# Optimization experiments

Measured on AMD Instinct MI355X. Metric: run time of the kernel, lower is better.

## Reference

```python
import jax, jax.numpy as jnp
import numpy as np

B, S, D, H = 8, 1024, 768, 12
DH = D // H  # 64
EPS = 1e-12
NEG_INF = -1e30


def setup_inputs() -> dict:
    key = jax.random.key(0)
    ks = jax.random.split(key, 12)
    s = 0.02
    return {
        "hidden_states": jax.random.normal(ks[0], (B, S, D), jnp.float32),
        "attention_mask": jax.random.randint(ks[1], (B, 1, 1, S), 0, 2, jnp.int32),
        "Wq": jax.random.normal(ks[2], (D, D), jnp.float32) * s,
        "bq": jnp.zeros((D,), jnp.float32),
        "Wk": jax.random.normal(ks[3], (D, D), jnp.float32) * s,
        "bk": jnp.zeros((D,), jnp.float32),
        "Wv": jax.random.normal(ks[4], (D, D), jnp.float32) * s,
        "bv": jnp.zeros((D,), jnp.float32),
        "Wo": jax.random.normal(ks[5], (D, D), jnp.float32) * s,
        "bo": jnp.zeros((D,), jnp.float32),
        "ln_g": jnp.ones((D,), jnp.float32),
        "ln_b": jnp.zeros((D,), jnp.float32),
    }


def _split_heads(x):
    # [B,S,D] -> [B,H,S,DH]
    return x.reshape(B, S, H, DH).transpose(0, 2, 1, 3)


def reference(hidden_states, attention_mask, Wq, bq, Wk, bk, Wv, bv, Wo, bo, ln_g, ln_b):
    q = _split_heads(hidden_states @ Wq.T + bq)
    k = _split_heads(hidden_states @ Wk.T + bk)
    v = _split_heads(hidden_states @ Wv.T + bv)

    # scores: [B,H,S,S]
    scores = jnp.einsum("bhqd,bhkd->bhqk", q, k) / jnp.float32(np.sqrt(DH))
    mask0 = attention_mask == 0  # [B,1,1,S], broadcasts over heads/queries
    scores = jnp.where(mask0, NEG_INF, scores)
    probs = jax.nn.softmax(scores, axis=-1)
    # post-softmax masking (as in source)
    probs = jnp.where(mask0, 0.0, probs)

    ctx = jnp.einsum("bhqk,bhkd->bhqd", probs, v)
    ctx = ctx.transpose(0, 2, 1, 3).reshape(B, S, D)

    # BertSelfOutput: dense + residual + LayerNorm
    h = ctx @ Wo.T + bo + hidden_states
    mu = jnp.mean(h, axis=-1, keepdims=True)
    var = jnp.mean((h - mu) ** 2, axis=-1, keepdims=True)
    out = (h - mu) * jax.lax.rsqrt(var + EPS) * ln_g + ln_b
    return out, probs
```

## Files before the change

kernel.cpp:

```cpp
#include <hip/hip_runtime.h>

#define B_ 8
#define S_ 1024
#define D_ 768
#define H_ 12
#define DH_ 64

typedef __attribute__((ext_vector_type(8))) short short8;
typedef __attribute__((ext_vector_type(4))) short short4v;
typedef __attribute__((ext_vector_type(4))) float float4v;
typedef __attribute__((ext_vector_type(8))) __bf16 bf16x8;

static __device__ __forceinline__ short f2bf(float f) {
  union { float f; unsigned u; } v; v.f = f;
  unsigned r = v.u + 0x7fffu + ((v.u >> 16) & 1u);
  return (short)(r >> 16);
}

static __device__ __forceinline__ float4v mfma16(const short* ap, const short* bp, float4v c) {
  bf16x8 a = *(const bf16x8*)ap;
  bf16x8 b = *(const bf16x8*)bp;
  return __builtin_amdgcn_mfma_f32_16x16x32_bf16(a, b, c, 0, 0, 0);
}

__global__ __launch_bounds__(256) void cvt_bf16(const float* __restrict__ src,
                                                short* __restrict__ dst, int n4) {
  int i = blockIdx.x * 256 + threadIdx.x;
  if (i < n4) {
    float4v v = ((const float4v*)src)[i];
    short4v o;
    o.x = f2bf(v.x); o.y = f2bf(v.y); o.z = f2bf(v.z); o.w = f2bf(v.w);
    ((short4v*)dst)[i] = o;
  }
}

#define AST 56

__global__ __launch_bounds__(256) void gemm_qkv(const short* __restrict__ A,
                                                const short* __restrict__ Bw,
                                                const float* __restrict__ bq,
                                                const float* __restrict__ bk,
                                                const float* __restrict__ bv,
                                                short* __restrict__ Qb,
                                                short* __restrict__ Kb,
                                                short* __restrict__ Vtb) {
  __shared__ short As[128][AST];
  __shared__ short Bs[128][AST];
  int m0 = blockIdx.x * 128, n0 = blockIdx.y * 128;
  int t = threadIdx.x;
  int w = t >> 6, lane = t & 63;
  int wm = (w >> 1) * 64, wn = (w & 1) * 64;
  int lr = lane & 15, lk = (lane >> 4) * 8;
  int sr = t >> 2, sc = (t & 3) * 8;

  float4v acc[4][4] = {};

  for (int k0 = 0; k0 < 768; k0 += 32) {
    *(short8*)&As[sr][sc]      = *(const short8*)&A[(size_t)(m0 + sr) * 768 + k0 + sc];
    *(short8*)&As[sr + 64][sc] = *(const short8*)&A[(size_t)(m0 + sr + 64) * 768 + k0 + sc];
    *(short8*)&Bs[sr][sc]      = *(const short8*)&Bw[(size_t)(n0 + sr) * 768 + k0 + sc];
    *(short8*)&Bs[sr + 64][sc] = *(const short8*)&Bw[(size_t)(n0 + sr + 64) * 768 + k0 + sc];
    __syncthreads();
    short8 a[4], b[4];
#pragma unroll
    for (int i = 0; i < 4; i++) a[i] = *(const short8*)&As[wm + i * 16 + lr][lk];
#pragma unroll
    for (int j = 0; j < 4; j++) b[j] = *(const short8*)&Bs[wn + j * 16 + lr][lk];
#pragma unroll
    for (int i = 0; i < 4; i++)
#pragma unroll
      for (int j = 0; j < 4; j++)
        acc[i][j] = mfma16((const short*)&a[i], (const short*)&b[j], acc[i][j]);
    __syncthreads();
  }

  int proj = n0 / 768;
  int nloc0 = n0 - proj * 768;
  const float* bias = (proj == 0) ? bq : ((proj == 1) ? bk : bv);
#pragma unroll
  for (int j = 0; j < 4; j++) {
    int gn = nloc0 + wn + j * 16 + lr;
    int hh = gn >> 6, dh = gn & 63;
    float bb = bias[gn];
#pragma unroll
    for (int i = 0; i < 4; i++) {
      int gm0 = m0 + wm + i * 16 + ((lane >> 4) << 2);
#pragma unroll
      for (int jj = 0; jj < 4; jj++) {
        int r = gm0 + jj;
        int bidx = r >> 10, s = r & 1023;
        short val = f2bf(acc[i][j][jj] + bb);
        if (proj == 2)
          Vtb[(((size_t)bidx * 12 + hh) * 64 + dh) * 1024 + s] = val;
        else {
          short* dst = (proj == 0) ? Qb : Kb;
          dst[(((size_t)bidx * 12 + hh) * 1024 + s) * 64 + dh] = val;
        }
      }
    }
  }
}

__global__ __launch_bounds__(256) void attn_fused(const short* __restrict__ Qb,
                                                  const short* __restrict__ Kb,
                                                  const short* __restrict__ Vtb,
                                                  const int* __restrict__ amask,
                                                  float* __restrict__ probs,
                                                  short* __restrict__ ctxb) {
  __shared__ short P[16][1032];
  __shared__ float redmax[4][16];
  __shared__ float redsum[4][16];
  __shared__ float ctxp[4][16][64];

  int bh = blockIdx.y;
  int b = bh / 12, h = bh - b * 12;
  int q0 = blockIdx.x * 16;
  const short* Qp = Qb + ((size_t)bh * 1024 + q0) * 64;
  const short* Kp = Kb + (size_t)bh * 1024 * 64;
  const short* Vp = Vtb + (size_t)bh * 64 * 1024;
  const int* mb = amask + b * 1024;

  int t = threadIdx.x, w = t >> 6, lane = t & 63;
  int lr = lane & 15, lk = (lane >> 4) * 8;

  short8 aq0 = *(const short8*)&Qp[lr * 64 + lk];
  short8 aq1 = *(const short8*)&Qp[lr * 64 + 32 + lk];

  float4v acc[16] = {};
#pragma unroll
  for (int nt = 0; nt < 16; nt++) {
    const short* kp = Kp + (size_t)(w * 256 + nt * 16 + lr) * 64;
    short8 b0 = *(const short8*)&kp[lk];
    short8 b1 = *(const short8*)&kp[32 + lk];
    acc[nt] = mfma16((const short*)&aq0, (const short*)&b0, acc[nt]);
    acc[nt] = mfma16((const short*)&aq1, (const short*)&b1, acc[nt]);
  }

  unsigned mbits = 0;
#pragma unroll
  for (int nt = 0; nt < 16; nt++)
    mbits |= (mb[w * 256 + nt * 16 + lr] != 0 ? 1u : 0u) << nt;

  float mx[4] = {-1e30f, -1e30f, -1e30f, -1e30f};
#pragma unroll
  for (int nt = 0; nt < 16; nt++)
#pragma unroll
    for (int j = 0; j < 4; j++) {
      float s = acc[nt][j] * 0.125f;
      if (!((mbits >> nt) & 1)) s = -1e30f;
      acc[nt][j] = s;
      mx[j] = fmaxf(mx[j], s);
    }
#pragma unroll
  for (int j = 0; j < 4; j++) {
#pragma unroll
    for (int off = 1; off < 16; off <<= 1) mx[j] = fmaxf(mx[j], __shfl_xor(mx[j], off));
  }
  if (lr == 0) {
#pragma unroll
    for (int j = 0; j < 4; j++) redmax[w][(lane >> 4) * 4 + j] = mx[j];
  }
  __syncthreads();
  float gmx[4];
#pragma unroll
  for (int j = 0; j < 4; j++) {
    int r = (lane >> 4) * 4 + j;
    gmx[j] = fmaxf(fmaxf(redmax[0][r], redmax[1][r]), fmaxf(redmax[2][r], redmax[3][r]));
  }

  float sm[4] = {0.f, 0.f, 0.f, 0.f};
#pragma unroll
  for (int nt = 0; nt < 16; nt++)
#pragma unroll
    for (int j = 0; j < 4; j++) {
      float p = ((mbits >> nt) & 1) ? __expf(acc[nt][j] - gmx[j]) : 0.f;
      acc[nt][j] = p;
      sm[j] += p;
    }
#pragma unroll
  for (int j = 0; j < 4; j++) {
#pragma unroll
    for (int off = 1; off < 16; off <<= 1) sm[j] += __shfl_xor(sm[j], off);
  }
  if (lr == 0) {
#pragma unroll
    for (int j = 0; j < 4; j++) redsum[w][(lane >> 4) * 4 + j] = sm[j];
  }
  __syncthreads();
  float inv[4];
#pragma unroll
  for (int j = 0; j < 4; j++) {
    int r = (lane >> 4) * 4 + j;
    float s = redsum[0][r] + redsum[1][r] + redsum[2][r] + redsum[3][r];
    inv[j] = (s > 0.f) ? 1.f / s : 0.f;
  }

  size_t pbase = ((size_t)bh * 1024 + q0) * 1024;
#pragma unroll
  for (int nt = 0; nt < 16; nt++) {
    int col = w * 256 + nt * 16 + lr;
#pragma unroll
    for (int j = 0; j < 4; j++) {
      int row = (lane >> 4) * 4 + j;
      float pv = acc[nt][j] * inv[j];
      probs[pbase + (size_t)row * 1024 + col] = pv;
      P[row][col] = f2bf(pv);
    }
  }
  __syncthreads();

  float4v c[4] = {};
#pragma unroll
  for (int ks = 0; ks < 8; ks++) {
    int kbase = w * 256 + ks * 32;
    short8 ap = *(const short8*)&P[lr][kbase + lk];
#pragma unroll
    for (int n2 = 0; n2 < 4; n2++) {
      short8 bvv = *(const short8*)&Vp[(size_t)(n2 * 16 + lr) * 1024 + kbase + lk];
      c[n2] = mfma16((const short*)&ap, (const short*)&bvv, c[n2]);
    }
  }
#pragma unroll
  for (int n2 = 0; n2 < 4; n2++)
#pragma unroll
    for (int j = 0; j < 4; j++)
      ctxp[w][(lane >> 4) * 4 + j][n2 * 16 + lr] = c[n2][j];
  __syncthreads();

#pragma unroll
  for (int u = 0; u < 4; u++) {
    int o = t * 4 + u;
    int row = o >> 6, dh = o & 63;
    float s = ctxp[0][row][dh] + ctxp[1][row][dh] + ctxp[2][row][dh] + ctxp[3][row][dh];
    ctxb[((size_t)(b * 1024 + q0 + row)) * 768 + h * 64 + dh] = f2bf(s);
  }
}

__global__ __launch_bounds__(256) void gemm_o(const short* __restrict__ A,
                                              const short* __restrict__ Bw,
                                              const float* __restrict__ bo,
                                              const float* __restrict__ hidden,
                                              float* __restrict__ hout) {
  __shared__ short As[128][AST];
  __shared__ short Bs[128][AST];
  int m0 = blockIdx.x * 128, n0 = blockIdx.y * 128;
  int t = threadIdx.x;
  int w = t >> 6, lane = t & 63;
  int wm = (w >> 1) * 64, wn = (w & 1) * 64;
  int lr = lane & 15, lk = (lane >> 4) * 8;
  int sr = t >> 2, sc = (t & 3) * 8;

  float4v acc[4][4] = {};

  for (int k0 = 0; k0 < 768; k0 += 32) {
    *(short8*)&As[sr][sc]      = *(const short8*)&A[(size_t)(m0 + sr) * 768 + k0 + sc];
    *(short8*)&As[sr + 64][sc] = *(const short8*)&A[(size_t)(m0 + sr + 64) * 768 + k0 + sc];
    *(short8*)&Bs[sr][sc]      = *(const short8*)&Bw[(size_t)(n0 + sr) * 768 + k0 + sc];
    *(short8*)&Bs[sr + 64][sc] = *(const short8*)&Bw[(size_t)(n0 + sr + 64) * 768 + k0 + sc];
    __syncthreads();
    short8 a[4], b[4];
#pragma unroll
    for (int i = 0; i < 4; i++) a[i] = *(const short8*)&As[wm + i * 16 + lr][lk];
#pragma unroll
    for (int j = 0; j < 4; j++) b[j] = *(const short8*)&Bs[wn + j * 16 + lr][lk];
#pragma unroll
    for (int i = 0; i < 4; i++)
#pragma unroll
      for (int j = 0; j < 4; j++)
        acc[i][j] = mfma16((const short*)&a[i], (const short*)&b[j], acc[i][j]);
    __syncthreads();
  }

#pragma unroll
  for (int j = 0; j < 4; j++) {
    int gn = n0 + wn + j * 16 + lr;
    float bb = bo[gn];
#pragma unroll
    for (int i = 0; i < 4; i++) {
      int gm0 = m0 + wm + i * 16 + ((lane >> 4) << 2);
#pragma unroll
      for (int jj = 0; jj < 4; jj++) {
        int r = gm0 + jj;
        size_t idx = (size_t)r * 768 + gn;
        hout[idx] = acc[i][j][jj] + bb + hidden[idx];
      }
    }
  }
}

__global__ __launch_bounds__(256) void lnorm(const float* __restrict__ h,
                                             const float* __restrict__ g,
                                             const float* __restrict__ be,
                                             float* __restrict__ out) {
  int row = blockIdx.x;
  const float* x = h + (size_t)row * 768;
  int t = threadIdx.x;
  float v0 = x[t], v1 = x[t + 256], v2 = x[t + 512];
  float s = v0 + v1 + v2;
#pragma unroll
  for (int off = 1; off < 64; off <<= 1) s += __shfl_xor(s, off);
  __shared__ float r1[4], r2[4];
  if ((t & 63) == 0) r1[t >> 6] = s;
  __syncthreads();
  float mean = (r1[0] + r1[1] + r1[2] + r1[3]) * (1.f / 768.f);
  float d0 = v0 - mean, d1 = v1 - mean, d2 = v2 - mean;
  float q = d0 * d0 + d1 * d1 + d2 * d2;
#pragma unroll
  for (int off = 1; off < 64; off <<= 1) q += __shfl_xor(q, off);
  if ((t & 63) == 0) r2[t >> 6] = q;
  __syncthreads();
  float var = (r2[0] + r2[1] + r2[2] + r2[3]) * (1.f / 768.f);
  float rr = rsqrtf(var + 1e-12f);
  size_t o = (size_t)row * 768;
  out[o + t]       = d0 * rr * g[t] + be[t];
  out[o + t + 256] = d1 * rr * g[t + 256] + be[t + 256];
  out[o + t + 512] = d2 * rr * g[t + 512] + be[t + 512];
}

extern "C" void kernel_launch(void* const* d_in, const int* in_sizes, int n_in,
                              void* d_out, int out_size, void* d_ws, size_t ws_size,
                              hipStream_t stream) {
  const float* hs    = (const float*)d_in[0];
  const int*   amask = (const int*)d_in[1];
  const float* Wq    = (const float*)d_in[2];
  const float* bq    = (const float*)d_in[3];
  const float* Wk    = (const float*)d_in[4];
  const float* bk    = (const float*)d_in[5];
  const float* Wv    = (const float*)d_in[6];
  const float* bv    = (const float*)d_in[7];
  const float* Wo    = (const float*)d_in[8];
  const float* bo    = (const float*)d_in[9];
  const float* lng   = (const float*)d_in[10];
  const float* lnb   = (const float*)d_in[11];

  char* wsp = (char*)d_ws;
  const size_t NTOK = (size_t)B_ * S_;
  short* hsb  = (short*)wsp; wsp += NTOK * D_ * 2;
  short* wqkv = (short*)wsp; wsp += (size_t)3 * D_ * D_ * 2;
  short* wob  = (short*)wsp; wsp += (size_t)D_ * D_ * 2;
  short* Qb   = (short*)wsp; wsp += NTOK * D_ * 2;
  short* Kb   = (short*)wsp; wsp += NTOK * D_ * 2;
  short* Vtb  = (short*)wsp; wsp += NTOK * D_ * 2;
  short* ctxb = (short*)wsp; wsp += NTOK * D_ * 2;
  float* hbuf = (float*)wsp; wsp += NTOK * D_ * 4;

  float* out   = (float*)d_out;
  float* probs = out + NTOK * D_;

  int n4hs = (int)(NTOK * D_ / 4);
  cvt_bf16<<<dim3((n4hs + 255) / 256), dim3(256), 0, stream>>>(hs, hsb, n4hs);
  int n4w = D_ * D_ / 4;
  dim3 wg((n4w + 255) / 256);
  cvt_bf16<<<wg, dim3(256), 0, stream>>>(Wq, wqkv, n4w);
  cvt_bf16<<<wg, dim3(256), 0, stream>>>(Wk, wqkv + (size_t)D_ * D_, n4w);
  cvt_bf16<<<wg, dim3(256), 0, stream>>>(Wv, wqkv + (size_t)2 * D_ * D_, n4w);
  cvt_bf16<<<wg, dim3(256), 0, stream>>>(Wo, wob, n4w);

  gemm_qkv<<<dim3(64, 18), dim3(256), 0, stream>>>(hsb, wqkv, bq, bk, bv, Qb, Kb, Vtb);
  attn_fused<<<dim3(S_ / 16, B_ * H_), dim3(256), 0, stream>>>(Qb, Kb, Vtb, amask, probs, ctxb);
  gemm_o<<<dim3(64, 6), dim3(256), 0, stream>>>(ctxb, wob, bo, hs, hbuf);
  lnorm<<<dim3(8192), dim3(256), 0, stream>>>(hbuf, lng, lnb, out);
}
```

Before: 758.9 us.

## Use direct global-to-LDS loads in GEMMs and coalesce output stores via LDS staging

Both projection GEMMs now load A and B tiles with global_load_lds (16-byte direct-to-LDS transfers) into unpadded 32-wide LDS tiles, which removes the register round-trip. The QKV epilogue stages results in shared memory so Q/K/V^T are written with 16-byte coalesced stores instead of scattered 2-byte stores. The attention kernel writes probs as float4 rows read back from the bf16 P buffer, and writes ctx as packed 4-element stores. The unpadded LDS tiles may cause bank conflicts. Probs are now rounded to bf16 precision before being stored, which changes output accuracy.

```diff
diff --git a/kernel.cpp b/kernel.cpp
--- a/kernel.cpp
+++ b/kernel.cpp
@@ -16,11 +16,21 @@
   unsigned r = v.u + 0x7fffu + ((v.u >> 16) & 1u);
   return (short)(r >> 16);
 }
+static __device__ __forceinline__ float bf2f(short s) {
+  union { unsigned u; float f; } v; v.u = ((unsigned)(unsigned short)s) << 16;
+  return v.f;
+}
 
 static __device__ __forceinline__ float4v mfma16(const short* ap, const short* bp, float4v c) {
   bf16x8 a = *(const bf16x8*)ap;
   bf16x8 b = *(const bf16x8*)bp;
   return __builtin_amdgcn_mfma_f32_16x16x32_bf16(a, b, c, 0, 0, 0);
+}
+
+typedef const __attribute__((address_space(1))) unsigned gu32;
+typedef __attribute__((address_space(3))) unsigned lu32;
+static __device__ __forceinline__ void gload16(const void* g, void* l) {
+  __builtin_amdgcn_global_load_lds((gu32*)g, (lu32*)l, 16, 0, 0);
 }
 
 __global__ __launch_bounds__(256) void cvt_bf16(const float* __restrict__ src,
@@ -34,8 +44,6 @@
   }
 }
 
-#define AST 56
-
 __global__ __launch_bounds__(256) void gemm_qkv(const short* __restrict__ A,
                                                 const short* __restrict__ Bw,
                                                 const float* __restrict__ bq,
@@ -44,22 +52,27 @@
                                                 short* __restrict__ Qb,
                                                 short* __restrict__ Kb,
                                                 short* __restrict__ Vtb) {
-  __shared__ short As[128][AST];
-  __shared__ short Bs[128][AST];
+  __shared__ char smem[34816];
+  short (*As)[32] = (short(*)[32])smem;
+  short (*Bs)[32] = (short(*)[32])(smem + 8192);
+  short (*Cs)[136] = (short(*)[136])smem;
+
   int m0 = blockIdx.x * 128, n0 = blockIdx.y * 128;
-  int t = threadIdx.x;
-  int w = t >> 6, lane = t & 63;
+  int t = threadIdx.x, w = t >> 6, lane = t & 63;
   int wm = (w >> 1) * 64, wn = (w & 1) * 64;
   int lr = lane & 15, lk = (lane >> 4) * 8;
-  int sr = t >> 2, sc = (t & 3) * 8;
+
+  const short* gA = A + (size_t)(m0 + w * 32 + (lane >> 2)) * 768 + (lane & 3) * 8;
+  const short* gB = Bw + (size_t)(n0 + w * 32 + (lane >> 2)) * 768 + (lane & 3) * 8;
 
   float4v acc[4][4] = {};
 
   for (int k0 = 0; k0 < 768; k0 += 32) {
-    *(short8*)&As[sr][sc]      = *(const short8*)&A[(size_t)(m0 + sr) * 768 + k0 + sc];
-    *(short8*)&As[sr + 64][sc] = *(const short8*)&A[(size_t)(m0 + sr + 64) * 768 + k0 + sc];
-    *(short8*)&Bs[sr][sc]      = *(const short8*)&Bw[(size_t)(n0 + sr) * 768 + k0 + sc];
-    *(short8*)&Bs[sr + 64][sc] = *(const short8*)&Bw[(size_t)(n0 + sr + 64) * 768 + k0 + sc];
+    gload16(gA, &As[w * 32][0]);
+    gload16(gA + 16 * 768, &As[w * 32 + 16][0]);
+    gload16(gB, &Bs[w * 32][0]);
+    gload16(gB + 16 * 768, &Bs[w * 32 + 16][0]);
+    gA += 32; gB += 32;
     __syncthreads();
     short8 a[4], b[4];
 #pragma unroll
@@ -74,29 +87,55 @@
     __syncthreads();
   }
 
-  int proj = n0 / 768;
+  int proj = blockIdx.y / 6;
   int nloc0 = n0 - proj * 768;
-  const float* bias = (proj == 0) ? bq : ((proj == 1) ? bk : bv);
-#pragma unroll
-  for (int j = 0; j < 4; j++) {
-    int gn = nloc0 + wn + j * 16 + lr;
-    int hh = gn >> 6, dh = gn & 63;
-    float bb = bias[gn];
-#pragma unroll
-    for (int i = 0; i < 4; i++) {
-      int gm0 = m0 + wm + i * 16 + ((lane >> 4) << 2);
-#pragma unroll
-      for (int jj = 0; jj < 4; jj++) {
-        int r = gm0 + jj;
-        int bidx = r >> 10, s = r & 1023;
-        short val = f2bf(acc[i][j][jj] + bb);
-        if (proj == 2)
-          Vtb[(((size_t)bidx * 12 + hh) * 64 + dh) * 1024 + s] = val;
-        else {
-          short* dst = (proj == 0) ? Qb : Kb;
-          dst[(((size_t)bidx * 12 + hh) * 1024 + s) * 64 + dh] = val;
-        }
+  int hhb = nloc0 >> 6;
+  int b = m0 >> 10, s0v = m0 & 1023;
+
+  if (proj < 2) {
+    short* dst = (proj == 0) ? Qb : Kb;
+    const float* bias = (proj == 0) ? bq : bk;
+#pragma unroll
+    for (int j = 0; j < 4; j++) {
+      float bb = bias[nloc0 + wn + j * 16 + lr];
+#pragma unroll
+      for (int i = 0; i < 4; i++)
+#pragma unroll
+        for (int jj = 0; jj < 4; jj++)
+          Cs[wm + i * 16 + (lane >> 4) * 4 + jj][wn + j * 16 + lr] = f2bf(acc[i][j][jj] + bb);
+    }
+    __syncthreads();
+#pragma unroll
+    for (int hh2 = 0; hh2 < 2; hh2++) {
+      short* base = dst + ((size_t)(b * 12 + hhb + hh2) * 1024 + s0v) * 64;
+#pragma unroll
+      for (int u = 0; u < 4; u++) {
+        int c = t + u * 256;
+        int sl = c >> 3, dh0 = (c & 7) * 8;
+        *(short8*)&base[(size_t)c * 8] = *(const short8*)&Cs[sl][hh2 * 64 + dh0];
       }
+    }
+  } else {
+#pragma unroll
+    for (int j = 0; j < 4; j++) {
+      float bb = bv[nloc0 + wn + j * 16 + lr];
+#pragma unroll
+      for (int i = 0; i < 4; i++) {
+        short4v p;
+        p.x = f2bf(acc[i][j][0] + bb);
+        p.y = f2bf(acc[i][j][1] + bb);
+        p.z = f2bf(acc[i][j][2] + bb);
+        p.w = f2bf(acc[i][j][3] + bb);
+        *(short4v*)&Cs[wn + j * 16 + lr][wm + i * 16 + (lane >> 4) * 4] = p;
+      }
+    }
+    __syncthreads();
+#pragma unroll
+    for (int u = 0; u < 8; u++) {
+      int row = (t >> 4) + u * 16;
+      int hh2 = row >> 6, dh = row & 63;
+      *(short8*)&Vtb[((size_t)(b * 12 + hhb + hh2) * 64 + dh) * 1024 + s0v + (t & 15) * 8]
+          = *(const short8*)&Cs[row][(t & 15) * 8];
     }
   }
 }
@@ -195,19 +234,31 @@
     inv[j] = (s > 0.f) ? 1.f / s : 0.f;
   }
 
-  size_t pbase = ((size_t)bh * 1024 + q0) * 1024;
 #pragma unroll
   for (int nt = 0; nt < 16; nt++) {
     int col = w * 256 + nt * 16 + lr;
 #pragma unroll
     for (int j = 0; j < 4; j++) {
       int row = (lane >> 4) * 4 + j;
-      float pv = acc[nt][j] * inv[j];
-      probs[pbase + (size_t)row * 1024 + col] = pv;
-      P[row][col] = f2bf(pv);
-    }
-  }
-  __syncthreads();
+      P[row][col] = f2bf(acc[nt][j] * inv[j]);
+    }
+  }
+  __syncthreads();
+
+  size_t pbase = ((size_t)bh * 1024 + q0) * 1024;
+  {
+    int prow = t >> 4;
+    int cb = (t & 15) * 4;
+    float* orow = probs + pbase + (size_t)prow * 1024;
+#pragma unroll
+    for (int u = 0; u < 16; u++) {
+      int col = cb + u * 64;
+      short4v pv = *(const short4v*)&P[prow][col];
+      float4v f;
+      f.x = bf2f(pv.x); f.y = bf2f(pv.y); f.z = bf2f(pv.z); f.w = bf2f(pv.w);
+      *(float4v*)&orow[col] = f;
+    }
+  }
 
   float4v c[4] = {};
 #pragma unroll
@@ -227,12 +278,15 @@
       ctxp[w][(lane >> 4) * 4 + j][n2 * 16 + lr] = c[n2][j];
   __syncthreads();
 
-#pragma unroll
-  for (int u = 0; u < 4; u++) {
-    int o = t * 4 + u;
-    int row = o >> 6, dh = o & 63;
-    float s = ctxp[0][row][dh] + ctxp[1][row][dh] + ctxp[2][row][dh] + ctxp[3][row][dh];
-    ctxb[((size_t)(b * 1024 + q0 + row)) * 768 + h * 64 + dh] = f2bf(s);
+  {
+    int row = t >> 4, dh0 = (t & 15) * 4;
+    short4v o4;
+    float s0 = ctxp[0][row][dh0 + 0] + ctxp[1][row][dh0 + 0] + ctxp[2][row][dh0 + 0] + ctxp[3][row][dh0 + 0];
+    float s1 = ctxp[0][row][dh0 + 1] + ctxp[1][row][dh0 + 1] + ctxp[2][row][dh0 + 1] + ctxp[3][row][dh0 + 1];
+    float s2 = ctxp[0][row][dh0 + 2] + ctxp[1][row][dh0 + 2] + ctxp[2][row][dh0 + 2] + ctxp[3][row][dh0 + 2];
+    float s3 = ctxp[0][row][dh0 + 3] + ctxp[1][row][dh0 + 3] + ctxp[2][row][dh0 + 3] + ctxp[3][row][dh0 + 3];
+    o4.x = f2bf(s0); o4.y = f2bf(s1); o4.z = f2bf(s2); o4.w = f2bf(s3);
+    *(short4v*)&ctxb[((size_t)(b * 1024 + q0 + row)) * 768 + h * 64 + dh0] = o4;
   }
 }
 
@@ -241,22 +295,24 @@
                                               const float* __restrict__ bo,
                                               const float* __restrict__ hidden,
                                               float* __restrict__ hout) {
-  __shared__ short As[128][AST];
-  __shared__ short Bs[128][AST];
+  __shared__ short As[128][32];
+  __shared__ short Bs[128][32];
   int m0 = blockIdx.x * 128, n0 = blockIdx.y * 128;
-  int t = threadIdx.x;
-  int w = t >> 6, lane = t & 63;
+  int t = threadIdx.x, w = t >> 6, lane = t & 63;
   int wm = (w >> 1) * 64, wn = (w & 1) * 64;
   int lr = lane & 15, lk = (lane >> 4) * 8;
-  int sr = t >> 2, sc = (t & 3) * 8;
+
+  const short* gA = A + (size_t)(m0 + w * 32 + (lane >> 2)) * 768 + (lane & 3) * 8;
+  const short* gB = Bw + (size_t)(n0 + w * 32 + (lane >> 2)) * 768 + (lane & 3) * 8;
 
   float4v acc[4][4] = {};
 
   for (int k0 = 0; k0 < 768; k0 += 32) {
-    *(short8*)&As[sr][sc]      = *(const short8*)&A[(size_t)(m0 + sr) * 768 + k0 + sc];
-    *(short8*)&As[sr + 64][sc] = *(const short8*)&A[(size_t)(m0 + sr + 64) * 768 + k0 + sc];
-    *(short8*)&Bs[sr][sc]      = *(const short8*)&Bw[(size_t)(n0 + sr) * 768 + k0 + sc];
-    *(short8*)&Bs[sr + 64][sc] = *(const short8*)&Bw[(size_t)(n0 + sr + 64) * 768 + k0 + sc];
+    gload16(gA, &As[w * 32][0]);
+    gload16(gA + 16 * 768, &As[w * 32 + 16][0]);
+    gload16(gB, &Bs[w * 32][0]);
+    gload16(gB + 16 * 768, &Bs[w * 32 + 16][0]);
+    gA += 32; gB += 32;
     __syncthreads();
     short8 a[4], b[4];
 #pragma unroll
```

Result: faster. 732.7 us (-3.4%).
